# Kernel optimization log

Hardware: AMD Instinct MI355X
Metric: run time of the kernel (lower is better)

The kernel has to match this reference:

```python
import jax, jax.numpy as jnp
import numpy as np

B, L, IN_DIM = 4, 2048, 1024
H, D = 16, 64
OUT_DIM = 1024


def setup_inputs() -> dict:
    key = jax.random.key(0)
    k1, k2, k3 = jax.random.split(key, 3)
    inputs = jax.random.normal(k1, (B, L, IN_DIM), dtype=jnp.float32)
    # nn.Linear weight init scale ~ 1/sqrt(fan_in); keep values moderate
    W_qkv = jax.random.normal(k2, (IN_DIM, 3 * H * D), dtype=jnp.float32) * (IN_DIM ** -0.5)
    W_out = jax.random.normal(k3, (H * D, OUT_DIM), dtype=jnp.float32) * ((H * D) ** -0.5)
    return {"inputs": inputs, "W_qkv": W_qkv, "W_out": W_out}


def reference(inputs, W_qkv, W_out):
    b, l, _ = inputs.shape
    qkv = inputs @ W_qkv                      # [B, L, 3*H*D]
    q, k, v = jnp.split(qkv, 3, axis=-1)
    q = q.reshape(b, l, H, D)
    k = k.reshape(b, l, H, D)
    v = v.reshape(b, l, H, D)
    score = jnp.einsum('bihd,bjhd->bijh', q, k) / (D ** 0.5)  # [B, L, L, H]
    # sequence_mask(arange(1..L)) == lower-triangular causal mask
    mask = jnp.tril(jnp.ones((l, l), dtype=score.dtype))[None, :, :, None]
    masked_score = score * mask + 1e30 * (mask - 1.0)
    wmat = jax.nn.softmax(masked_score, axis=2)
    out = jnp.einsum('bijh,bjhd->bihd', wmat, v).reshape(b, l, H * D)
    return out @ W_out
```

## Files before the change

### kernel.cpp

```cpp
#include <hip/hip_runtime.h>

#define DEVI __device__ __forceinline__

typedef __attribute__((ext_vector_type(8))) short bh8;
typedef __attribute__((ext_vector_type(4))) float f32x4;

static constexpr int Bsz  = 4;
static constexpr int Lseq = 2048;
static constexpr int INDIM = 1024;
static constexpr int NH = 16;
static constexpr int HD = 64;
static constexpr int QKVN = 3 * NH * HD;
static constexpr int OUTD = 1024;
static constexpr int Mrows = Bsz * Lseq;

DEVI unsigned short f2bf(float f) {
    unsigned u = __float_as_uint(f);
    u = u + 0x7fffu + ((u >> 16) & 1u);
    return (unsigned short)(u >> 16);
}

DEVI void gl2lds16(const unsigned short* g, unsigned short* l) {
    __builtin_amdgcn_global_load_lds(
        (const __attribute__((address_space(1))) void*)g,
        (__attribute__((address_space(3))) void*)l, 16, 0, 0);
}

__global__ __launch_bounds__(256) void convert_f32_bf16(
    const float* __restrict__ in, unsigned short* __restrict__ out, int n8) {
    int i = blockIdx.x * 256 + threadIdx.x;
    if (i >= n8) return;
    const f32x4* p = (const f32x4*)(in + (size_t)i * 8);
    f32x4 a = p[0], b = p[1];
    bh8 o;
    o[0] = (short)f2bf(a[0]); o[1] = (short)f2bf(a[1]);
    o[2] = (short)f2bf(a[2]); o[3] = (short)f2bf(a[3]);
    o[4] = (short)f2bf(b[0]); o[5] = (short)f2bf(b[1]);
    o[6] = (short)f2bf(b[2]); o[7] = (short)f2bf(b[3]);
    *(bh8*)(out + (size_t)i * 8) = o;
}

__global__ __launch_bounds__(256) void transpose_f32_bf16(
    const float* __restrict__ W, unsigned short* __restrict__ Wt, int K, int N) {
    __shared__ unsigned short t[64][65];
    int n0 = blockIdx.x * 64, k0 = blockIdx.y * 64;
    int tid = threadIdx.x;
#pragma unroll
    for (int i = 0; i < 16; ++i) {
        int idx = tid + i * 256;
        int r = idx >> 6, c = idx & 63;
        t[r][c] = f2bf(W[(size_t)(k0 + r) * N + (n0 + c)]);
    }
    __syncthreads();
#pragma unroll
    for (int i = 0; i < 16; ++i) {
        int idx = tid + i * 256;
        int r = idx >> 6, c = idx & 63;
        Wt[(size_t)(n0 + r) * K + (k0 + c)] = t[c][r];
    }
}

template <int MODE>
__global__ __launch_bounds__(256) void gemm_bt(
    const unsigned short* __restrict__ A, const unsigned short* __restrict__ Bt,
    float* __restrict__ Cf, unsigned short* __restrict__ Qg,
    unsigned short* __restrict__ Kg, unsigned short* __restrict__ Vg,
    int K, int ntn, int cpx) {
    __shared__ unsigned short Al[2][128 * 32];
    __shared__ unsigned short Bl[2][128 * 32];
    int tid = threadIdx.x;
    int lane = tid & 63, wave = tid >> 6;
    int bid = blockIdx.x;
    int swz = (bid & 7) * cpx + (bid >> 3);
    int mt = swz / ntn, nt_ = swz % ntn;
    int m0 = mt * 128, n0 = nt_ * 128;
    int wm = (wave >> 1) * 64, wn = (wave & 1) * 64;

    int srow = tid >> 2;
    int skof = (tid & 3) * 8;
    const unsigned short* Ags = A + (size_t)(m0 + srow) * K + skof;
    const unsigned short* Bgs = Bt + (size_t)(n0 + srow) * K + skof;
    int wofs = wave * 512;

    f32x4 acc[4][4] = {};
    int cl = lane & 15, kq = (lane >> 4) * 8;

    int nt = K >> 5;
    gl2lds16(Ags, &Al[0][0] + wofs);
    gl2lds16(Ags + (size_t)64 * K, &Al[0][0] + 2048 + wofs);
    gl2lds16(Bgs, &Bl[0][0] + wofs);
    gl2lds16(Bgs + (size_t)64 * K, &Bl[0][0] + 2048 + wofs);
    __syncthreads();

    int cur = 0;
    for (int t = 0; t < nt; ++t) {
        if (t + 1 < nt) {
            int k1 = (t + 1) * 32;
            gl2lds16(Ags + k1, &Al[cur ^ 1][0] + wofs);
            gl2lds16(Ags + (size_t)64 * K + k1, &Al[cur ^ 1][0] + 2048 + wofs);
            gl2lds16(Bgs + k1, &Bl[cur ^ 1][0] + wofs);
            gl2lds16(Bgs + (size_t)64 * K + k1, &Bl[cur ^ 1][0] + 2048 + wofs);
        }
        bh8 af[4], bf[4];
#pragma unroll
        for (int mi = 0; mi < 4; ++mi)
            af[mi] = *(const bh8*)(&Al[cur][0] + (wm + mi * 16 + cl) * 32 + kq);
#pragma unroll
        for (int nj = 0; nj < 4; ++nj)
            bf[nj] = *(const bh8*)(&Bl[cur][0] + (wn + nj * 16 + cl) * 32 + kq);
#pragma unroll
        for (int mi = 0; mi < 4; ++mi)
#pragma unroll
            for (int nj = 0; nj < 4; ++nj)
                acc[mi][nj] = __builtin_amdgcn_mfma_f32_16x16x32_bf16(
                    af[mi], bf[nj], acc[mi][nj], 0, 0, 0);
        if (t + 1 < nt) __syncthreads();
        cur ^= 1;
    }

    int rb = (lane >> 4) * 4;
#pragma unroll
    for (int mi = 0; mi < 4; ++mi) {
#pragma unroll
        for (int nj = 0; nj < 4; ++nj) {
#pragma unroll
            for (int r = 0; r < 4; ++r) {
                int gm = m0 + wm + mi * 16 + rb + r;
                int gn = n0 + wn + nj * 16 + cl;
                float v = acc[mi][nj][r];
                if (MODE == 0) {
                    int b = gm >> 11, ls = gm & 2047;
                    int sel = gn >> 10, h = (gn >> 6) & 15, d = gn & 63;
                    if (sel == 0)
                        Qg[((size_t)(b * NH + h) * Lseq + ls) * HD + d] = f2bf(v * 0.125f);
                    else if (sel == 1)
                        Kg[((size_t)(b * NH + h) * Lseq + ls) * HD + d] = f2bf(v);
                    else
                        Vg[((size_t)(b * NH + h) * HD + d) * Lseq + ls] = f2bf(v);
                } else {
                    Cf[(size_t)gm * OUTD + gn] = v;
                }
            }
        }
    }
}

__global__ __launch_bounds__(256) void attn_causal(
    const unsigned short* __restrict__ Qg, const unsigned short* __restrict__ Kg,
    const unsigned short* __restrict__ Vt, unsigned short* __restrict__ Og) {
    __shared__ unsigned short Kl[64 * 64];
    __shared__ unsigned short Vl[64 * 64];
    __shared__ unsigned short Pl[4][16 * 72];
    int tid = threadIdx.x, wave = tid >> 6, lane = tid & 63;
    int bid = blockIdx.x;
    int xcd = bid & 7, slot = bid >> 3;
    int p = slot & 15;
    int bh = ((slot >> 4) << 3) | xcd;
    int b = bh >> 4, h = bh & 15;
    const unsigned short* Qp = Qg + (size_t)bh * Lseq * HD;
    const unsigned short* Kp = Kg + (size_t)bh * Lseq * HD;
    const unsigned short* Vp = Vt + (size_t)bh * HD * Lseq;
    int cl = lane & 15, kq = (lane >> 4) * 8, rb = (lane >> 4) * 4;
    unsigned short* Pw = &Pl[wave][0];

    int srow = tid >> 2;
    int sc0 = (tid & 3) * 16;
    int ssw = (srow & 7) << 3;

    bh8 ones;
#pragma unroll
    for (int i = 0; i < 8; ++i) ones[i] = (short)0x3F80;

    for (int pass = 0; pass < 2; ++pass) {
        int pt = pass ? (31 - p) : p;
        int q0 = pt * 64 + wave * 16;

        bh8 qf0 = *(const bh8*)(Qp + (size_t)(q0 + cl) * HD + kq);
        bh8 qf1 = *(const bh8*)(Qp + (size_t)(q0 + cl) * HD + 32 + kq);

        f32x4 o[4] = {};
        f32x4 osum = {};

        int nblk = pt + 1;
        for (int j = 0; j < nblk; ++j) {
            int kv0 = j * 64;
            const unsigned short* Ks = Kp + (size_t)(kv0 + srow) * HD;
            const unsigned short* Vs = Vp + (size_t)srow * Lseq + kv0;
            bh8 k0 = *(const bh8*)(Ks + sc0);
            bh8 k1 = *(const bh8*)(Ks + sc0 + 8);
            bh8 v0 = *(const bh8*)(Vs + sc0);
            bh8 v1 = *(const bh8*)(Vs + sc0 + 8);
            __syncthreads();
            *(bh8*)(Kl + srow * 64 + (sc0 ^ ssw)) = k0;
            *(bh8*)(Kl + srow * 64 + ((sc0 + 8) ^ ssw)) = k1;
            *(bh8*)(Vl + srow * 64 + (sc0 ^ ssw)) = v0;
            *(bh8*)(Vl + srow * 64 + ((sc0 + 8) ^ ssw)) = v1;
            __syncthreads();
            __builtin_amdgcn_s_setprio(1);
#pragma unroll
            for (int nb = 0; nb < 4; ++nb) {
                int row = nb * 16 + cl, rs = (row & 7) << 3;
                bh8 kf0 = *(const bh8*)(Kl + row * 64 + (kq ^ rs));
                bh8 kf1 = *(const bh8*)(Kl + row * 64 + ((kq + 32) ^ rs));
                f32x4 s = {};
                s = __builtin_amdgcn_mfma_f32_16x16x32_bf16(qf0, kf0, s, 0, 0, 0);
                s = __builtin_amdgcn_mfma_f32_16x16x32_bf16(qf1, kf1, s, 0, 0, 0);
                int col = kv0 + nb * 16 + cl;
#pragma unroll
                for (int r = 0; r < 4; ++r) {
                    float v = s[r];
                    if (col > q0 + rb + r) v = -3e30f;
                    Pw[(rb + r) * 72 + nb * 16 + cl] = f2bf(__expf(v));
                }
            }
            bh8 pa0 = *(const bh8*)(Pw + cl * 72 + kq);
            bh8 pa1 = *(const bh8*)(Pw + cl * 72 + 32 + kq);
#pragma unroll
            for (int db = 0; db < 4; ++db) {
                int dr = db * 16 + cl, ds = (dr & 7) << 3;
                bh8 vf0 = *(const bh8*)(Vl + dr * 64 + (kq ^ ds));
                bh8 vf1 = *(const bh8*)(Vl + dr * 64 + ((kq + 32) ^ ds));
                o[db] = __builtin_amdgcn_mfma_f32_16x16x32_bf16(pa0, vf0, o[db], 0, 0, 0);
                o[db] = __builtin_amdgcn_mfma_f32_16x16x32_bf16(pa1, vf1, o[db], 0, 0, 0);
            }
            osum = __builtin_amdgcn_mfma_f32_16x16x32_bf16(pa0, ones, osum, 0, 0, 0);
            osum = __builtin_amdgcn_mfma_f32_16x16x32_bf16(pa1, ones, osum, 0, 0, 0);
            __builtin_amdgcn_s_setprio(0);
        }
#pragma unroll
        for (int r = 0; r < 4; ++r) {
            float inv = 1.0f / osum[r];
            int row = q0 + rb + r;
            size_t obase = (size_t)(b * Lseq + row) * OUTD + h * HD;
#pragma unroll
            for (int db = 0; db < 4; ++db)
                Og[obase + db * 16 + cl] = f2bf(o[db][r] * inv);
        }
    }
}

extern "C" void kernel_launch(void* const* d_in, const int* in_sizes, int n_in,
                              void* d_out, int out_size, void* d_ws, size_t ws_size,
                              hipStream_t stream) {
    (void)in_sizes; (void)n_in; (void)out_size; (void)ws_size;
    const float* X    = (const float*)d_in[0];
    const float* Wqkv = (const float*)d_in[1];
    const float* Wout = (const float*)d_in[2];
    float* out = (float*)d_out;

    char* ws = (char*)d_ws;
    size_t off = 0;
    unsigned short* Xb    = (unsigned short*)(ws + off); off += (size_t)Mrows * INDIM * 2;
    unsigned short* WqkvT = (unsigned short*)(ws + off); off += (size_t)QKVN * INDIM * 2;
    unsigned short* WoutT = (unsigned short*)(ws + off); off += (size_t)OUTD * (NH * HD) * 2;
    unsigned short* Qg    = (unsigned short*)(ws + off); off += (size_t)Mrows * NH * HD * 2;
    unsigned short* Kg    = (unsigned short*)(ws + off); off += (size_t)Mrows * NH * HD * 2;
    unsigned short* Vtg   = (unsigned short*)(ws + off); off += (size_t)Mrows * NH * HD * 2;
    unsigned short* Ob    = (unsigned short*)(ws + off); off += (size_t)Mrows * NH * HD * 2;

    convert_f32_bf16<<<(Mrows * INDIM / 8 + 255) / 256, 256, 0, stream>>>(
        X, Xb, Mrows * INDIM / 8);
    transpose_f32_bf16<<<dim3(QKVN / 64, INDIM / 64), 256, 0, stream>>>(
        Wqkv, WqkvT, INDIM, QKVN);
    transpose_f32_bf16<<<dim3(OUTD / 64, (NH * HD) / 64), 256, 0, stream>>>(
        Wout, WoutT, NH * HD, OUTD);
    gemm_bt<0><<<(Mrows / 128) * (QKVN / 128), 256, 0, stream>>>(
        Xb, WqkvT, nullptr, Qg, Kg, Vtg, INDIM, QKVN / 128,
        (Mrows / 128) * (QKVN / 128) / 8);
    attn_causal<<<Bsz * NH * 16, 256, 0, stream>>>(Qg, Kg, Vtg, Ob);
    gemm_bt<1><<<(Mrows / 128) * (OUTD / 128), 256, 0, stream>>>(
        Ob, WoutT, out, nullptr, nullptr, nullptr, NH * HD, OUTD / 128,
        (Mrows / 128) * (OUTD / 128) / 8);
}
```

Measured before the change: 205.1 us.

## Double GEMM K-tile to 64 and XOR-swizzle LDS layout

The bf16 GEMM kernel now stages 64-wide K tiles instead of 32, which halves the number of barrier-separated iterations and doubles the MFMA work per sync. The LDS tile is stored with an XOR swizzle on the 8-element column chunk, keyed by row, to reduce bank conflicts on the fragment reads. LDS use per block doubles to 64 KB, which may lower occupancy.

```diff
diff --git a/kernel.cpp b/kernel.cpp
--- a/kernel.cpp
+++ b/kernel.cpp
@@ -66,8 +66,8 @@
     float* __restrict__ Cf, unsigned short* __restrict__ Qg,
     unsigned short* __restrict__ Kg, unsigned short* __restrict__ Vg,
     int K, int ntn, int cpx) {
-    __shared__ unsigned short Al[2][128 * 32];
-    __shared__ unsigned short Bl[2][128 * 32];
+    __shared__ unsigned short Al[2][128 * 64];
+    __shared__ unsigned short Bl[2][128 * 64];
     int tid = threadIdx.x;
     int lane = tid & 63, wave = tid >> 6;
     int bid = blockIdx.x;
@@ -76,44 +76,54 @@
     int m0 = mt * 128, n0 = nt_ * 128;
     int wm = (wave >> 1) * 64, wn = (wave & 1) * 64;
 
-    int srow = tid >> 2;
-    int skof = (tid & 3) * 8;
-    const unsigned short* Ags = A + (size_t)(m0 + srow) * K + skof;
-    const unsigned short* Bgs = Bt + (size_t)(n0 + srow) * K + skof;
+    int srow = tid >> 3;
+    int scol = ((tid & 7) ^ (srow & 7)) * 8;
+    const unsigned short* Ags = A + (size_t)(m0 + srow) * K + scol;
+    const unsigned short* Bgs = Bt + (size_t)(n0 + srow) * K + scol;
     int wofs = wave * 512;
 
     f32x4 acc[4][4] = {};
     int cl = lane & 15, kq = (lane >> 4) * 8;
 
-    int nt = K >> 5;
-    gl2lds16(Ags, &Al[0][0] + wofs);
-    gl2lds16(Ags + (size_t)64 * K, &Al[0][0] + 2048 + wofs);
-    gl2lds16(Bgs, &Bl[0][0] + wofs);
-    gl2lds16(Bgs + (size_t)64 * K, &Bl[0][0] + 2048 + wofs);
+    int nt = K >> 6;
+    auto stage = [&](int t, int buf) {
+        int kof = t * 64;
+#pragma unroll
+        for (int i = 0; i < 4; ++i) {
+            gl2lds16(Ags + (size_t)(32 * i) * K + kof, &Al[buf][0] + 32 * i * 64 + wofs);
+            gl2lds16(Bgs + (size_t)(32 * i) * K + kof, &Bl[buf][0] + 32 * i * 64 + wofs);
+        }
+    };
+
+    stage(0, 0);
     __syncthreads();
 
     int cur = 0;
     for (int t = 0; t < nt; ++t) {
-        if (t + 1 < nt) {
-            int k1 = (t + 1) * 32;
-            gl2lds16(Ags + k1, &Al[cur ^ 1][0] + wofs);
-            gl2lds16(Ags + (size_t)64 * K + k1, &Al[cur ^ 1][0] + 2048 + wofs);
-            gl2lds16(Bgs + k1, &Bl[cur ^ 1][0] + wofs);
-            gl2lds16(Bgs + (size_t)64 * K + k1, &Bl[cur ^ 1][0] + 2048 + wofs);
-        }
-        bh8 af[4], bf[4];
-#pragma unroll
-        for (int mi = 0; mi < 4; ++mi)
-            af[mi] = *(const bh8*)(&Al[cur][0] + (wm + mi * 16 + cl) * 32 + kq);
-#pragma unroll
-        for (int nj = 0; nj < 4; ++nj)
-            bf[nj] = *(const bh8*)(&Bl[cur][0] + (wn + nj * 16 + cl) * 32 + kq);
-#pragma unroll
-        for (int mi = 0; mi < 4; ++mi)
-#pragma unroll
-            for (int nj = 0; nj < 4; ++nj)
-                acc[mi][nj] = __builtin_amdgcn_mfma_f32_16x16x32_bf16(
-                    af[mi], bf[nj], acc[mi][nj], 0, 0, 0);
+        if (t + 1 < nt) stage(t + 1, cur ^ 1);
+        bh8 af[4][2], bf[4][2];
+#pragma unroll
+        for (int mi = 0; mi < 4; ++mi) {
+            int ar = wm + mi * 16 + cl, as = (ar & 7) << 3;
+#pragma unroll
+            for (int ks = 0; ks < 2; ++ks)
+                af[mi][ks] = *(const bh8*)(&Al[cur][0] + ar * 64 + ((ks * 32 + kq) ^ as));
+        }
+#pragma unroll
+        for (int nj = 0; nj < 4; ++nj) {
+            int br = wn + nj * 16 + cl, bs = (br & 7) << 3;
+#pragma unroll
+            for (int ks = 0; ks < 2; ++ks)
+                bf[nj][ks] = *(const bh8*)(&Bl[cur][0] + br * 64 + ((ks * 32 + kq) ^ bs));
+        }
+#pragma unroll
+        for (int ks = 0; ks < 2; ++ks)
+#pragma unroll
+            for (int mi = 0; mi < 4; ++mi)
+#pragma unroll
+                for (int nj = 0; nj < 4; ++nj)
+                    acc[mi][nj] = __builtin_amdgcn_mfma_f32_16x16x32_bf16(
+                        af[mi][ks], bf[nj][ks], acc[mi][nj], 0, 0, 0);
         if (t + 1 < nt) __syncthreads();
         cur ^= 1;
     }
```

After: 198.3 us (median of 2 runs). 1.03x faster.
